# Kernel tuning notes

Hardware: AMD Instinct MI355X
Metric: run time of the kernel (lower is better)

## Reference

```python
import jax, jax.numpy as jnp
import numpy as np
from jax import lax

V, H, L_ENC, L_DEC = 32000, 1024, 2, 2
B, T_ENC, T_DEC = 32, 128, 128


def lstm_layer(x, W, U, b, h0, c0):
    """Keras-style LSTM. x: [B,T,H], W:[H,4H], U:[H,4H], b:[4H]. Gate order i,f,g,o."""
    xz = jnp.einsum('bth,hg->btg', x, W) + b  # precompute input projections [B,T,4H]

    def step(carry, z_t):
        h, c = carry
        z = z_t + h @ U  # [B,4H]
        i, f, g, o = jnp.split(z, 4, axis=-1)
        c = jax.nn.sigmoid(f) * c + jax.nn.sigmoid(i) * jnp.tanh(g)
        h = jax.nn.sigmoid(o) * jnp.tanh(c)
        return (h, c), h

    (hT, cT), hs = lax.scan(step, (h0, c0), jnp.swapaxes(xz, 0, 1))
    return jnp.swapaxes(hs, 0, 1), hT, cT


def setup_inputs() -> dict:
    key = jax.random.key(0)
    ks = jax.random.split(key, 12)
    s = 0.05
    return {
        'encoder_tokens': jax.random.randint(ks[0], (B, T_ENC), 0, V),
        'decoder_tokens': jax.random.randint(ks[1], (B, T_DEC), 0, V),
        'emb': jax.random.normal(ks[2], (V, H), jnp.float32) * s,
        'enc_W': jax.random.normal(ks[3], (L_ENC, H, 4 * H), jnp.float32) * s,
        'enc_U': jax.random.normal(ks[4], (L_ENC, H, 4 * H), jnp.float32) * s,
        'enc_b': jnp.zeros((L_ENC, 4 * H), jnp.float32),
        'dec_W': jax.random.normal(ks[5], (L_DEC, H, 4 * H), jnp.float32) * s,
        'dec_U': jax.random.normal(ks[6], (L_DEC, H, 4 * H), jnp.float32) * s,
        'dec_b': jnp.zeros((L_DEC, 4 * H), jnp.float32),
        'dense_W': jax.random.normal(ks[7], (H, V), jnp.float32) * s,
        'dense_b': jnp.zeros((V,), jnp.float32),
    }


def reference(encoder_tokens, decoder_tokens, emb, enc_W, enc_U, enc_b,
              dec_W, dec_U, dec_b, dense_W, dense_b):
    b = encoder_tokens.shape[0]
    x = emb[encoder_tokens]  # [B,T,H]; dropout is identity at inference
    y = emb[decoder_tokens]
    h = jnp.zeros((b, H), x.dtype)
    c = jnp.zeros((b, H), x.dtype)
    # states thread layer -> next layer, encoder -> decoder (as in source)
    for l in range(enc_W.shape[0]):
        x, h, c = lstm_layer(x, enc_W[l], enc_U[l], enc_b[l], h, c)
    for l in range(dec_W.shape[0]):
        y, h, c = lstm_layer(y, dec_W[l], dec_U[l], dec_b[l], h, c)
    return y[:, -1, :] @ dense_W + dense_b  # [B,V]
```

## Files before the change

### kernel.cpp

```cpp
#include <hip/hip_runtime.h>
#include <cstdint>
#include <cstddef>


#define H_    1024
#define G4H   4096
#define B_    32
#define T_    128
#define BT_   4096
#define V_    32000

typedef unsigned short u16;
typedef __attribute__((ext_vector_type(8))) short   short8;
typedef __attribute__((ext_vector_type(8))) __bf16  bf16x8;
typedef __attribute__((ext_vector_type(4))) float   f32x4;

__device__ __forceinline__ u16 f2bf(float f) {
  unsigned u = __float_as_uint(f);
  u += 0x7fffu + ((u >> 16) & 1u);
  return (u16)(u >> 16);
}
__device__ __forceinline__ float bf2f(u16 s) {
  return __uint_as_float(((unsigned)s) << 16);
}
__device__ __forceinline__ f32x4 MF(short8 a, short8 b, f32x4 c) {
  return __builtin_amdgcn_mfma_f32_16x16x32_bf16(
      __builtin_bit_cast(bf16x8, a), __builtin_bit_cast(bf16x8, b), c, 0, 0, 0);
}
__device__ __forceinline__ void g2lds16(const void* g, void* l) {
  __builtin_amdgcn_global_load_lds(
      (const __attribute__((address_space(1))) unsigned int*)g,
      (__attribute__((address_space(3))) unsigned int*)l, 16, 0, 0);
}

__device__ __forceinline__ void gbar(unsigned* cnt, unsigned* gen) {
  __syncthreads();
  if (threadIdx.x == 0) {
    __threadfence();
    unsigned g = __hip_atomic_load(gen, __ATOMIC_RELAXED, __HIP_MEMORY_SCOPE_AGENT);
    unsigned a = __hip_atomic_fetch_add(cnt, 1u, __ATOMIC_ACQ_REL, __HIP_MEMORY_SCOPE_AGENT);
    if (a == gridDim.x - 1) {
      __hip_atomic_store(cnt, 0u, __ATOMIC_RELAXED, __HIP_MEMORY_SCOPE_AGENT);
      __hip_atomic_fetch_add(gen, 1u, __ATOMIC_RELEASE, __HIP_MEMORY_SCOPE_AGENT);
    } else {
      while (__hip_atomic_load(gen, __ATOMIC_ACQUIRE, __HIP_MEMORY_SCOPE_AGENT) == g)
        __builtin_amdgcn_s_sleep(2);
    }
    __threadfence();
  }
  __syncthreads();
}

__global__ __launch_bounds__(256) void k_embed(
    const int* __restrict__ etok, const int* __restrict__ dtok,
    const float* __restrict__ emb,
    u16* __restrict__ xh, u16* __restrict__ xl,
    u16* __restrict__ yh, u16* __restrict__ yl) {
  int tid  = blockIdx.x * 256 + threadIdx.x;
  int half = tid >> 19;
  int loc  = tid & 524287;
  int row  = loc >> 7;
  int kap  = loc & 127;
  int tok  = half ? dtok[row] : etok[row];
  const float* src = emb + (size_t)tok * H_ + kap * 8;
  u16* dh = half ? yh : xh;
  u16* dl = half ? yl : xl;
  int b = row >> 7, t = row & 127;
  size_t off = ((size_t)(b * 128 + kap) * 128 + t) * 8;
  unsigned hi[4], lo[4];
#pragma unroll
  for (int p = 0; p < 4; ++p) {
    float v0 = src[2 * p], v1 = src[2 * p + 1];
    u16 h0 = f2bf(v0), h1 = f2bf(v1);
    u16 l0 = f2bf(v0 - bf2f(h0)), l1 = f2bf(v1 - bf2f(h1));
    hi[p] = (unsigned)h0 | ((unsigned)h1 << 16);
    lo[p] = (unsigned)l0 | ((unsigned)l1 << 16);
  }
  *(uint4*)(dh + off) = make_uint4(hi[0], hi[1], hi[2], hi[3]);
  *(uint4*)(dl + off) = make_uint4(lo[0], lo[1], lo[2], lo[3]);
}

__global__ __launch_bounds__(256) void k_convW(
    const float* __restrict__ W, u16* __restrict__ bh, u16* __restrict__ bl) {
  int tid = blockIdx.x * 256 + threadIdx.x;
  int c = tid & 127, kap = (tid >> 7) & 127, nb = tid >> 14;
  int n = nb * 128 + c;
  unsigned hi[4], lo[4];
#pragma unroll
  for (int p = 0; p < 4; ++p) {
    float v0 = W[(size_t)(8 * kap + 2 * p) * G4H + n];
    float v1 = W[(size_t)(8 * kap + 2 * p + 1) * G4H + n];
    u16 h0 = f2bf(v0), h1 = f2bf(v1);
    u16 l0 = f2bf(v0 - bf2f(h0)), l1 = f2bf(v1 - bf2f(h1));
    hi[p] = (unsigned)h0 | ((unsigned)h1 << 16);
    lo[p] = (unsigned)l0 | ((unsigned)l1 << 16);
  }
  size_t off = ((size_t)(nb * 128 + kap) * 128 + c) * 8;
  *(uint4*)(bh + off) = make_uint4(hi[0], hi[1], hi[2], hi[3]);
  *(uint4*)(bl + off) = make_uint4(lo[0], lo[1], lo[2], lo[3]);
}

__global__ __launch_bounds__(256) void k_convU(
    const float* __restrict__ U, u16* __restrict__ uh, u16* __restrict__ ul) {
  int tid = blockIdx.x * 256 + threadIdx.x;
  int col = tid & 4095, kap = tid >> 12;
  unsigned hi[4], lo[4];
#pragma unroll
  for (int p = 0; p < 4; ++p) {
    float v0 = U[(size_t)(8 * kap + 2 * p) * G4H + col];
    float v1 = U[(size_t)(8 * kap + 2 * p + 1) * G4H + col];
    u16 h0 = f2bf(v0), h1 = f2bf(v1);
    u16 l0 = f2bf(v0 - bf2f(h0)), l1 = f2bf(v1 - bf2f(h1));
    hi[p] = (unsigned)h0 | ((unsigned)h1 << 16);
    lo[p] = (unsigned)l0 | ((unsigned)l1 << 16);
  }
  size_t off = ((size_t)col * 128 + kap) * 8;
  *(uint4*)(uh + off) = make_uint4(hi[0], hi[1], hi[2], hi[3]);
  *(uint4*)(ul + off) = make_uint4(lo[0], lo[1], lo[2], lo[3]);
}

__global__ __launch_bounds__(256) void k_gemm(
    const u16* __restrict__ Ah, const u16* __restrict__ Al,
    const u16* __restrict__ Bh, const u16* __restrict__ Bl,
    const float* __restrict__ bias, float* __restrict__ C) {
  __shared__ u16 lds[16384];
  int bm = blockIdx.x >> 5, bn = blockIdx.x & 31;
  int tid = threadIdx.x, lane = tid & 63, wv = tid >> 6;
  int wm = wv >> 1, wn = wv & 1;
  int kl = lane >> 4, rr = lane & 15;
  const f32x4 fz = {0.f, 0.f, 0.f, 0.f};
  f32x4 acc[4][4];
#pragma unroll
  for (int i = 0; i < 4; ++i)
#pragma unroll
    for (int j = 0; j < 4; ++j) acc[i][j] = fz;

  const u16* sbase = (wv == 0) ? Ah : (wv == 1) ? Al : (wv == 2) ? Bh : Bl;
  int blkidx = (wv < 2) ? bm : bn;
  u16* ldst = &lds[wv * 4096];

  for (int kt = 0; kt < 32; ++kt) {
    __syncthreads();
    const u16* src = sbase + ((size_t)(blkidx * 128 + kt * 4) * 128) * 8;
#pragma unroll
    for (int i = 0; i < 8; ++i)
      g2lds16(src + i * 512 + lane * 8, ldst + i * 512);
    asm volatile("s_waitcnt vmcnt(0)" ::: "memory");
    __syncthreads();

    short8 af[2][4], bf[2][4];
#pragma unroll
    for (int mi = 0; mi < 4; ++mi) {
      int o = (kl * 128 + wm * 64 + mi * 16 + rr) * 8;
      af[0][mi] = *(const short8*)&lds[o];
      af[1][mi] = *(const short8*)&lds[4096 + o];
    }
#pragma unroll
    for (int ni = 0; ni < 4; ++ni) {
      int o = (kl * 128 + wn * 64 + ni * 16 + rr) * 8;
      bf[0][ni] = *(const short8*)&lds[8192 + o];
      bf[1][ni] = *(const short8*)&lds[12288 + o];
    }
#pragma unroll
    for (int mi = 0; mi < 4; ++mi)
#pragma unroll
      for (int ni = 0; ni < 4; ++ni) {
        acc[mi][ni] = MF(af[0][mi], bf[0][ni], acc[mi][ni]);
        acc[mi][ni] = MF(af[0][mi], bf[1][ni], acc[mi][ni]);
        acc[mi][ni] = MF(af[1][mi], bf[0][ni], acc[mi][ni]);
      }
  }
#pragma unroll
  for (int ni = 0; ni < 4; ++ni) {
    int col = bn * 128 + wn * 64 + ni * 16 + rr;
    float bv = bias[col];
#pragma unroll
    for (int mi = 0; mi < 4; ++mi) {
      int row0 = bm * 128 + wm * 64 + mi * 16 + kl * 4;
#pragma unroll
      for (int j = 0; j < 4; ++j)
        C[(size_t)(row0 + j) * G4H + col] = acc[mi][ni][j] + bv;
    }
  }
}

__global__ __launch_bounds__(128) void k_scan(
    const u16* __restrict__ Uph, const u16* __restrict__ Upl,
    const float* __restrict__ xz,
    u16* __restrict__ h0h, u16* __restrict__ h0l,
    u16* __restrict__ h1h, u16* __restrict__ h1l,
    float* __restrict__ hf32, float* __restrict__ cstate,
    u16* __restrict__ hsH, u16* __restrict__ hsL,
    unsigned* cnt, unsigned* gen) {
  __shared__ u16 Us[32768];
  const int G = blockIdx.x;
  const int tid = threadIdx.x;
  const int lane = tid & 63;
  const int m = tid >> 6;
  const int kl = lane >> 4;
  const int c = lane & 15;
  const int q = c >> 2;
  const int uuc = c & 3;
  const int u = 4 * G + uuc;
  const int kap_u = u >> 3;
  const int e_u = u & 7;
  const int bb0 = m * 16 + c;

#pragma unroll
  for (int i = 0; i < 32; ++i) {
    int kb = i * 4;
    int kapl = kb + kl;
    int coll = q * H_ + 4 * G + uuc;
    const u16* gsrc = (m ? Upl : Uph) + ((size_t)coll * 128 + kapl) * 8;
    g2lds16(gsrc, &Us[m * 16384 + kb * 128]);
  }
  asm volatile("s_waitcnt vmcnt(0)" ::: "memory");
  __syncthreads();

  float cst[4];
#pragma unroll
  for (int j = 0; j < 4; ++j)
    cst[j] = cstate[(size_t)(m * 16 + 4 * kl + j) * H_ + u];

  const f32x4 fz = {0.f, 0.f, 0.f, 0.f};
#pragma unroll 1
  for (int t = 0; t < T_; ++t) {
    const int rb = t & 1;
    const u16* hh = rb ? h1h : h0h;
    const u16* hl = rb ? h1l : h0l;
    u16* whh = rb ? h0h : h1h;
    u16* whl = rb ? h0l : h1l;

    float xzv[4];
#pragma unroll
    for (int j = 0; j < 4; ++j) {
      int bb = m * 16 + 4 * kl + j;
      xzv[j] = xz[(size_t)(bb * 128 + t) * G4H + q * H_ + 4 * G + uuc];
    }

    f32x4 av[4] = {fz, fz, fz, fz};
#pragma unroll
    for (int ks = 0; ks < 32; ++ks) {
      int kap = ks * 4 + kl;
      short8 ah = *(const short8*)&hh[((size_t)kap * 32 + bb0) * 8];
      short8 al = *(const short8*)&hl[((size_t)kap * 32 + bb0) * 8];
      short8 bh = *(const short8*)&Us[kap * 128 + c * 8];
      short8 bl = *(const short8*)&Us[16384 + kap * 128 + c * 8];
      av[ks & 3] = MF(ah, bh, av[ks & 3]);
      av[ks & 3] = MF(ah, bl, av[ks & 3]);
      av[ks & 3] = MF(al, bh, av[ks & 3]);
    }
    f32x4 zs = av[0] + av[1] + av[2] + av[3];

    float nl[4];
#pragma unroll
    for (int j = 0; j < 4; ++j) {
      float z = zs[j] + xzv[j];
      float s = (q == 2) ? 2.f * z : z;
      float sg = 1.f / (1.f + __expf(-s));
      nl[j] = (q == 2) ? (2.f * sg - 1.f) : sg;
    }
    int base = lane & 48;
    int lf = base | (4 + uuc), lg_ = base | (8 + uuc), lo_ = base | (12 + uuc);
#pragma unroll
    for (int j = 0; j < 4; ++j) {
      float fv = __shfl(nl[j], lf, 64);
      float gv = __shfl(nl[j], lg_, 64);
      float ov = __shfl(nl[j], lo_, 64);
      if (c < 4) {
        float cn = fv * cst[j] + nl[j] * gv;
        cst[j] = cn;
        float e2 = __expf(-2.f * cn);
        float hv = ov * ((1.f - e2) / (1.f + e2));
        int bb = m * 16 + 4 * kl + j;
        u16 hb = f2bf(hv);
        u16 lb = f2bf(hv - bf2f(hb));
        whh[((size_t)kap_u * 32 + bb) * 8 + e_u] = hb;
        whl[((size_t)kap_u * 32 + bb) * 8 + e_u] = lb;
        hf32[(size_t)bb * H_ + u] = hv;
        if (hsH != nullptr) {
          size_t ho = ((size_t)(bb * 128 + kap_u) * 128 + t) * 8 + e_u;
          hsH[ho] = hb;
          hsL[ho] = lb;
        }
      }
    }
    if (t != T_ - 1) gbar(cnt, gen);
  }
  if (c < 4) {
#pragma unroll
    for (int j = 0; j < 4; ++j)
      cstate[(size_t)(m * 16 + 4 * kl + j) * H_ + u] = cst[j];
  }
}

__global__ __launch_bounds__(256) void k_dense(
    const float* __restrict__ hf, const float* __restrict__ Wd,
    const float* __restrict__ bd, float* __restrict__ out) {
  __shared__ float hs_l[32][64];
  int tid = threadIdx.x;
  int v = blockIdx.x * 256 + tid;
  float acc[32];
#pragma unroll
  for (int b = 0; b < 32; ++b) acc[b] = 0.f;
  for (int kc = 0; kc < 16; ++kc) {
    __syncthreads();
    {
      int b = tid >> 3, k0 = (tid & 7) * 8;
      const float* s = &hf[(size_t)b * H_ + kc * 64 + k0];
      *(float4*)&hs_l[b][k0] = *(const float4*)s;
      *(float4*)&hs_l[b][k0 + 4] = *(const float4*)(s + 4);
    }
    __syncthreads();
#pragma unroll 4
    for (int k4 = 0; k4 < 16; ++k4) {
      float w0 = Wd[(size_t)(kc * 64 + k4 * 4 + 0) * V_ + v];
      float w1 = Wd[(size_t)(kc * 64 + k4 * 4 + 1) * V_ + v];
      float w2 = Wd[(size_t)(kc * 64 + k4 * 4 + 2) * V_ + v];
      float w3 = Wd[(size_t)(kc * 64 + k4 * 4 + 3) * V_ + v];
#pragma unroll
      for (int b = 0; b < 32; ++b) {
        float4 hv = *(const float4*)&hs_l[b][k4 * 4];
        acc[b] += hv.x * w0 + hv.y * w1 + hv.z * w2 + hv.w * w3;
      }
    }
  }
#pragma unroll
  for (int b = 0; b < 32; ++b)
    out[(size_t)b * V_ + v] = acc[b] + bd[v];
}

static const size_t OFF_CNT = 0;
static const size_t OFF_GEN = 64;
static const size_t OFF_CST = 256;
static const size_t OFF_H0H = OFF_CST + 131072;
static const size_t OFF_H0L = OFF_H0H + 65536;
static const size_t INIT_BYTES = OFF_H0L + 65536;
static const size_t OFF_H1H = INIT_BYTES;
static const size_t OFF_H1L = OFF_H1H + 65536;
static const size_t OFF_HF  = OFF_H1L + 65536;
static const size_t OFF_XZ  = OFF_HF + 131072;
static const size_t OFF_XEH = OFF_XZ + 67108864;
static const size_t OFF_XEL = OFF_XEH + 8388608;
static const size_t OFF_YDH = OFF_XEL + 8388608;
static const size_t OFF_YDL = OFF_YDH + 8388608;
static const size_t OFF_HSH = OFF_YDL + 8388608;
static const size_t OFF_HSL = OFF_HSH + 8388608;
static const size_t OFF_WPH = OFF_HSL + 8388608;
static const size_t OFF_WPL = OFF_WPH + 8388608;
static const size_t OFF_UPH = OFF_WPL + 8388608;
static const size_t OFF_UPL = OFF_UPH + 8388608;
static const size_t WS_NEED = OFF_UPL + 8388608;

extern "C" void kernel_launch(void* const* d_in, const int* in_sizes, int n_in,
                              void* d_out, int out_size, void* d_ws, size_t ws_size,
                              hipStream_t stream) {
  if (ws_size < WS_NEED) return;
  const int*   etok = (const int*)d_in[0];
  const int*   dtok = (const int*)d_in[1];
  const float* emb  = (const float*)d_in[2];
  const float* encW = (const float*)d_in[3];
  const float* encU = (const float*)d_in[4];
  const float* encB = (const float*)d_in[5];
  const float* decW = (const float*)d_in[6];
  const float* decU = (const float*)d_in[7];
  const float* decB = (const float*)d_in[8];
  const float* dW   = (const float*)d_in[9];
  const float* dB   = (const float*)d_in[10];
  float* out = (float*)d_out;
  char* ws = (char*)d_ws;

  unsigned* cnt = (unsigned*)(ws + OFF_CNT);
  unsigned* gen = (unsigned*)(ws + OFF_GEN);
  float* cstate = (float*)(ws + OFF_CST);
  u16* h0h = (u16*)(ws + OFF_H0H);
  u16* h0l = (u16*)(ws + OFF_H0L);
  u16* h1h = (u16*)(ws + OFF_H1H);
  u16* h1l = (u16*)(ws + OFF_H1L);
  float* hf32 = (float*)(ws + OFF_HF);
  float* xz   = (float*)(ws + OFF_XZ);
  u16* xEh = (u16*)(ws + OFF_XEH);
  u16* xEl = (u16*)(ws + OFF_XEL);
  u16* yDh = (u16*)(ws + OFF_YDH);
  u16* yDl = (u16*)(ws + OFF_YDL);
  u16* hsH = (u16*)(ws + OFF_HSH);
  u16* hsL = (u16*)(ws + OFF_HSL);
  u16* Wph = (u16*)(ws + OFF_WPH);
  u16* Wpl = (u16*)(ws + OFF_WPL);
  u16* Uph = (u16*)(ws + OFF_UPH);
  u16* Upl = (u16*)(ws + OFF_UPL);

  hipMemsetAsync(ws, 0, INIT_BYTES, stream);

  k_embed<<<4096, 256, 0, stream>>>(etok, dtok, emb, xEh, xEl, yDh, yDl);

  for (int l = 0; l < 4; ++l) {
    const float* Wsrc = (l < 2) ? encW + (size_t)l * H_ * G4H : decW + (size_t)(l - 2) * H_ * G4H;
    const float* Usrc = (l < 2) ? encU + (size_t)l * H_ * G4H : decU + (size_t)(l - 2) * H_ * G4H;
    const float* bsrc = (l < 2) ? encB + (size_t)l * G4H      : decB + (size_t)(l - 2) * G4H;
    const u16* Ah = (l == 0) ? xEh : (l == 2) ? yDh : hsH;
    const u16* Al = (l == 0) ? xEl : (l == 2) ? yDl : hsL;
    bool emit = (l == 0 || l == 2);

    k_convW<<<2048, 256, 0, stream>>>(Wsrc, Wph, Wpl);
    k_gemm<<<1024, 256, 0, stream>>>(Ah, Al, Wph, Wpl, bsrc, xz);
    k_convU<<<2048, 256, 0, stream>>>(Usrc, Uph, Upl);
    k_scan<<<256, 128, 0, stream>>>(Uph, Upl, xz, h0h, h0l, h1h, h1l, hf32, cstate,
                                    emit ? hsH : nullptr, emit ? hsL : nullptr,
                                    cnt, gen);
  }
  k_dense<<<125, 256, 0, stream>>>(hf32, dW, dB, out);
}
```

Baseline: 17.73 ms.

## Replace counter grid barrier with per-block step flags and transpose xz layout

```diff
diff --git a/kernel.cpp b/kernel.cpp
--- a/kernel.cpp
+++ b/kernel.cpp
@@ -33,21 +33,19 @@
       (__attribute__((address_space(3))) unsigned int*)l, 16, 0, 0);
 }
 
-__device__ __forceinline__ void gbar(unsigned* cnt, unsigned* gen) {
+__device__ __forceinline__ void gbarf(unsigned* flags, unsigned stepval) {
   __syncthreads();
-  if (threadIdx.x == 0) {
-    __threadfence();
-    unsigned g = __hip_atomic_load(gen, __ATOMIC_RELAXED, __HIP_MEMORY_SCOPE_AGENT);
-    unsigned a = __hip_atomic_fetch_add(cnt, 1u, __ATOMIC_ACQ_REL, __HIP_MEMORY_SCOPE_AGENT);
-    if (a == gridDim.x - 1) {
-      __hip_atomic_store(cnt, 0u, __ATOMIC_RELAXED, __HIP_MEMORY_SCOPE_AGENT);
-      __hip_atomic_fetch_add(gen, 1u, __ATOMIC_RELEASE, __HIP_MEMORY_SCOPE_AGENT);
-    } else {
-      while (__hip_atomic_load(gen, __ATOMIC_ACQUIRE, __HIP_MEMORY_SCOPE_AGENT) == g)
-        __builtin_amdgcn_s_sleep(2);
-    }
-    __threadfence();
-  }
+  if (threadIdx.x == 0)
+    __hip_atomic_store(&flags[blockIdx.x], stepval, __ATOMIC_RELEASE,
+                       __HIP_MEMORY_SCOPE_AGENT);
+  unsigned* f = flags + 2 * threadIdx.x;
+  for (;;) {
+    unsigned a = __hip_atomic_load(&f[0], __ATOMIC_RELAXED, __HIP_MEMORY_SCOPE_AGENT);
+    unsigned b = __hip_atomic_load(&f[1], __ATOMIC_RELAXED, __HIP_MEMORY_SCOPE_AGENT);
+    if (__all((a >= stepval) & (b >= stepval))) break;
+    __builtin_amdgcn_s_sleep(1);
+  }
+  __threadfence();
   __syncthreads();
 }
 
@@ -122,7 +120,7 @@
 __global__ __launch_bounds__(256) void k_gemm(
     const u16* __restrict__ Ah, const u16* __restrict__ Al,
     const u16* __restrict__ Bh, const u16* __restrict__ Bl,
-    const float* __restrict__ bias, float* __restrict__ C) {
+    const float* __restrict__ bias, float* __restrict__ xzT) {
   __shared__ u16 lds[16384];
   int bm = blockIdx.x >> 5, bn = blockIdx.x & 31;
   int tid = threadIdx.x, lane = tid & 63, wv = tid >> 6;
@@ -178,20 +176,23 @@
     for (int mi = 0; mi < 4; ++mi) {
       int row0 = bm * 128 + wm * 64 + mi * 16 + kl * 4;
 #pragma unroll
-      for (int j = 0; j < 4; ++j)
-        C[(size_t)(row0 + j) * G4H + col] = acc[mi][ni][j] + bv;
+      for (int j = 0; j < 4; ++j) {
+        int row = row0 + j;
+        int bb = row >> 7, tt = row & 127;
+        xzT[((size_t)tt * G4H + col) * 32 + bb] = acc[mi][ni][j] + bv;
+      }
     }
   }
 }
 
 __global__ __launch_bounds__(128) void k_scan(
     const u16* __restrict__ Uph, const u16* __restrict__ Upl,
-    const float* __restrict__ xz,
+    const float* __restrict__ xzT,
     u16* __restrict__ h0h, u16* __restrict__ h0l,
     u16* __restrict__ h1h, u16* __restrict__ h1l,
     float* __restrict__ hf32, float* __restrict__ cstate,
     u16* __restrict__ hsH, u16* __restrict__ hsL,
-    unsigned* cnt, unsigned* gen) {
+    unsigned* flags, unsigned sbase) {
   __shared__ u16 Us[32768];
   const int G = blockIdx.x;
   const int tid = threadIdx.x;
@@ -205,6 +206,7 @@
   const int kap_u = u >> 3;
   const int e_u = u & 7;
   const int bb0 = m * 16 + c;
+  const bool emit = (hsH != nullptr);
 
 #pragma unroll
   for (int i = 0; i < 32; ++i) {
@@ -231,12 +233,8 @@
     u16* whh = rb ? h0h : h1h;
     u16* whl = rb ? h0l : h1l;
 
-    float xzv[4];
-#pragma unroll
-    for (int j = 0; j < 4; ++j) {
-      int bb = m * 16 + 4 * kl + j;
-      xzv[j] = xz[(size_t)(bb * 128 + t) * G4H + q * H_ + 4 * G + uuc];
-    }
+    const float4 xv = *(const float4*)&xzT[
+        ((size_t)t * G4H + q * H_ + 4 * G + uuc) * 32 + m * 16 + 4 * kl];
 
     f32x4 av[4] = {fz, fz, fz, fz};
 #pragma unroll
@@ -253,6 +251,7 @@
     f32x4 zs = av[0] + av[1] + av[2] + av[3];
 
     float nl[4];
+    const float xzv[4] = {xv.x, xv.y, xv.z, xv.w};
 #pragma unroll
     for (int j = 0; j < 4; ++j) {
       float z = zs[j] + xzv[j];
@@ -277,15 +276,15 @@
         u16 lb = f2bf(hv - bf2f(hb));
         whh[((size_t)kap_u * 32 + bb) * 8 + e_u] = hb;
         whl[((size_t)kap_u * 32 + bb) * 8 + e_u] = lb;
-        hf32[(size_t)bb * H_ + u] = hv;
-        if (hsH != nullptr) {
+        if (t == T_ - 1) hf32[(size_t)bb * H_ + u] = hv;
+        if (emit) {
           size_t ho = ((size_t)(bb * 128 + kap_u) * 128 + t) * 8 + e_u;
           hsH[ho] = hb;
           hsL[ho] = lb;
         }
       }
     }
-    if (t != T_ - 1) gbar(cnt, gen);
+    if (t != T_ - 1) gbarf(flags, sbase + t + 1);
   }
   if (c < 4) {
 #pragma unroll
@@ -330,9 +329,8 @@
     out[(size_t)b * V_ + v] = acc[b] + bd[v];
 }
 
-static const size_t OFF_CNT = 0;
-static const size_t OFF_GEN = 64;
-static const size_t OFF_CST = 256;
+static const size_t OFF_FLG = 0;
+static const size_t OFF_CST = 1024;
 static const size_t OFF_H0H = OFF_CST + 131072;
 static const size_t OFF_H0L = OFF_H0H + 65536;
 static const size_t INIT_BYTES = OFF_H0L + 65536;
@@ -370,15 +368,14 @@
   float* out = (float*)d_out;
   char* ws = (char*)d_ws;
 
-  unsigned* cnt = (unsigned*)(ws + OFF_CNT);
-  unsigned* gen = (unsigned*)(ws + OFF_GEN);
+  unsigned* flags = (unsigned*)(ws + OFF_FLG);
   float* cstate = (float*)(ws + OFF_CST);
   u16* h0h = (u16*)(ws + OFF_H0H);
   u16* h0l = (u16*)(ws + OFF_H0L);
   u16* h1h = (u16*)(ws + OFF_H1H);
   u16* h1l = (u16*)(ws + OFF_H1L);
   float* hf32 = (float*)(ws + OFF_HF);
-  float* xz   = (float*)(ws + OFF_XZ);
+  float* xzT  = (float*)(ws + OFF_XZ);
   u16* xEh = (u16*)(ws + OFF_XEH);
   u16* xEl = (u16*)(ws + OFF_XEL);
   u16* yDh = (u16*)(ws + OFF_YDH);
@@ -403,11 +400,11 @@
     bool emit = (l == 0 || l == 2);
 
     k_convW<<<2048, 256, 0, stream>>>(Wsrc, Wph, Wpl);
-    k_gemm<<<1024, 256, 0, stream>>>(Ah, Al, Wph, Wpl, bsrc, xz);
+    k_gemm<<<1024, 256, 0, stream>>>(Ah, Al, Wph, Wpl, bsrc, xzT);
     k_convU<<<2048, 256, 0, stream>>>(Usrc, Uph, Upl);
-    k_scan<<<256, 128, 0, stream>>>(Uph, Upl, xz, h0h, h0l, h1h, h1l, hf32, cstate,
+    k_scan<<<256, 128, 0, stream>>>(Uph, Upl, xzT, h0h, h0l, h1h, h1l, hf32, cstate,
                                     emit ? hsH : nullptr, emit ? hsL : nullptr,
-                                    cnt, gen);
+                                    flags, (unsigned)(l * 128));
   }
   k_dense<<<125, 256, 0, stream>>>(hf32, dW, dB, out);
 }
```

New measurement: 15.11 ms. -14.8%, faster.
